# Performance work log

Hardware: AMD Instinct MI355X
Metric: run time of the kernel (lower is better)

The kernel has to match this reference:

```python
import jax, jax.numpy as jnp
import numpy as np

B, CIN, COUT, K, H, W = 16, 128, 256, 3, 56, 56
STRIDE = 1
PAD = K // 2


def setup_inputs() -> dict:
    key = jax.random.key(0)
    ks = jax.random.split(key, 12)
    x = jax.random.normal(ks[0], (B, CIN, H, W), dtype=jnp.float32)
    base_kernel = jax.random.normal(ks[1], (COUT, CIN, K, K), dtype=jnp.float32)
    bias = jnp.zeros((COUT,), dtype=jnp.float32)
    s = 1.0 / np.sqrt(CIN)
    fc_spatial_w = jax.random.uniform(ks[2], (K * K, CIN), minval=-s, maxval=s)
    fc_spatial_b = jax.random.uniform(ks[3], (K * K,), minval=-s, maxval=s)
    fc_in_w = jax.random.uniform(ks[4], (CIN, CIN), minval=-s, maxval=s)
    fc_in_b = jax.random.uniform(ks[5], (CIN,), minval=-s, maxval=s)
    fc_out_w = jax.random.uniform(ks[6], (COUT, CIN), minval=-s, maxval=s)
    fc_out_b = jax.random.uniform(ks[7], (COUT,), minval=-s, maxval=s)
    fc_kernel_w = jax.random.uniform(ks[8], (COUT * CIN * K * K, CIN), minval=-s, maxval=s)
    fc_kernel_b = jax.random.uniform(ks[9], (COUT * CIN * K * K,), minval=-s, maxval=s)
    return {
        "x": x, "base_kernel": base_kernel, "bias": bias,
        "fc_spatial_w": fc_spatial_w, "fc_spatial_b": fc_spatial_b,
        "fc_in_w": fc_in_w, "fc_in_b": fc_in_b,
        "fc_out_w": fc_out_w, "fc_out_b": fc_out_b,
        "fc_kernel_w": fc_kernel_w, "fc_kernel_b": fc_kernel_b,
    }


def _odconv(x, base_kernel, bias, fc_spatial_w, fc_spatial_b, fc_in_w, fc_in_b,
            fc_out_w, fc_out_b, fc_kernel_w, fc_kernel_b):
    b = x.shape[0]
    # global average pool -> context [B, Cin]
    context = jnp.mean(x, axis=(2, 3))
    sig = jax.nn.sigmoid
    attn_spatial = sig(context @ fc_spatial_w.T + fc_spatial_b).reshape(b, 1, 1, K, K)
    attn_in = sig(context @ fc_in_w.T + fc_in_b).reshape(b, 1, CIN, 1, 1)
    attn_out = sig(context @ fc_out_w.T + fc_out_b).reshape(b, COUT, 1, 1, 1)
    attn_kernel = sig(context @ fc_kernel_w.T + fc_kernel_b).reshape(b, COUT, CIN, K, K)
    # 5-way broadcast multiply -> per-sample dynamic kernel [B, Cout, Cin, K, K]
    dyn = base_kernel[None] * attn_out * attn_in * attn_spatial * attn_kernel

    def conv_one(xi, wi):
        # xi: [Cin, H, W], wi: [Cout, Cin, K, K]
        out = jax.lax.conv_general_dilated(
            xi[None], wi,
            window_strides=(STRIDE, STRIDE),
            padding=[(PAD, PAD), (PAD, PAD)],
            dimension_numbers=("NCHW", "OIHW", "NCHW"),
        )
        return out[0]

    out = jax.vmap(conv_one)(x, dyn)  # [B, Cout, H', W']
    return out + bias[None, :, None, None]


def reference(x, base_kernel, bias, fc_spatial_w, fc_spatial_b, fc_in_w, fc_in_b,
              fc_out_w, fc_out_b, fc_kernel_w, fc_kernel_b):
    return _odconv(x, base_kernel, bias, fc_spatial_w, fc_spatial_b, fc_in_w, fc_in_b,
                   fc_out_w, fc_out_b, fc_kernel_w, fc_kernel_b)
```

## Files before the change

kernel.cpp:

```cpp
#include <hip/hip_runtime.h>
#include <hip/hip_bf16.h>
#include <math.h>

#define BATCH 16
#define CIN   128
#define COUT  256
#define HH    56
#define WW    56
#define HW    3136
#define NTAP  9
#define NE    (COUT*CIN*NTAP)

typedef short short8 __attribute__((ext_vector_type(8)));
typedef float floatx4 __attribute__((ext_vector_type(4)));

#define WSB_CTX   0
#define WSB_ASP   8192
#define WSB_AIN   9472
#define WSB_AOUT  17664
#define WSB_ZP    34048
#define WSB_XT    38144
#define WSB_DYN   (WSB_XT + BATCH*HW*CIN*2)

static __device__ inline unsigned short f2b(float f) {
    union { float f; unsigned u; } v; v.f = f;
    unsigned r = v.u + 0x7FFF + ((v.u >> 16) & 1);
    return (unsigned short)(r >> 16);
}
static __device__ inline short8 pack8(float4 a, float4 b) {
    short8 r;
    r[0] = (short)f2b(a.x); r[1] = (short)f2b(a.y); r[2] = (short)f2b(a.z); r[3] = (short)f2b(a.w);
    r[4] = (short)f2b(b.x); r[5] = (short)f2b(b.y); r[6] = (short)f2b(b.z); r[7] = (short)f2b(b.w);
    return r;
}

typedef const __attribute__((address_space(1))) void* gas_ptr;
typedef __attribute__((address_space(3))) void* las_ptr;
static __device__ __forceinline__ void gl_lds16(const void* g, void* l) {
    __builtin_amdgcn_global_load_lds((gas_ptr)g, (las_ptr)l, 16, 0, 0);
}

__global__ void k_context(const float* __restrict__ x, float* __restrict__ ctx,
                          float* __restrict__ zp) {
    int bc = blockIdx.x;
    if (bc == 0 && threadIdx.x < 64) {
        uint4 z = {0u, 0u, 0u, 0u};
        ((uint4*)zp)[threadIdx.x] = z;
    }
    const float4* p = (const float4*)(x + (size_t)bc * HW);
    float s = 0.f;
    for (int i = threadIdx.x; i < HW / 4; i += 256) { float4 v = p[i]; s += v.x + v.y + v.z + v.w; }
    for (int off = 32; off; off >>= 1) s += __shfl_down(s, off, 64);
    __shared__ float red[4];
    if ((threadIdx.x & 63) == 0) red[threadIdx.x >> 6] = s;
    __syncthreads();
    if (threadIdx.x == 0) ctx[bc] = (red[0] + red[1] + red[2] + red[3]) * (1.f / (float)HW);
}

__global__ void k_attn(const float* __restrict__ ctx,
                       const float* __restrict__ wsp, const float* __restrict__ bsp,
                       const float* __restrict__ win, const float* __restrict__ bin,
                       const float* __restrict__ wout, const float* __restrict__ bout,
                       float* __restrict__ asp, float* __restrict__ ain, float* __restrict__ aout) {
    int R = blockIdx.x * 4 + (threadIdx.x >> 6);
    int lane = threadIdx.x & 63;
    int b = R / 393, r = R % 393;
    const float* w; float bias; float* o;
    if (r < 9)        { w = wsp  + r * CIN;         bias = bsp[r];         o = asp  + b * 16  + r; }
    else if (r < 137) { w = win  + (r - 9) * CIN;   bias = bin[r - 9];     o = ain  + b * CIN + (r - 9); }
    else              { w = wout + (r - 137) * CIN; bias = bout[r - 137];  o = aout + b * COUT + (r - 137); }
    float2 wv = ((const float2*)w)[lane];
    float2 cv = ((const float2*)(ctx + b * CIN))[lane];
    float d = wv.x * cv.x + wv.y * cv.y;
    for (int off = 32; off; off >>= 1) d += __shfl_down(d, off, 64);
    if (lane == 0) *o = 1.f / (1.f + __expf(-(d + bias)));
}

#define XT_BLOCKS    784
#define BUILD_BLOCKS 1152
__global__ void k_fat(const float* __restrict__ x, unsigned short* __restrict__ xt,
                      const float* __restrict__ ctx, const float* __restrict__ wk,
                      const float* __restrict__ bk, const float* __restrict__ base,
                      const float* __restrict__ asp, const float* __restrict__ ain,
                      const float* __restrict__ aout, unsigned short* __restrict__ dyn) {
    if (blockIdx.x < XT_BLOCKS) {
        int bid = blockIdx.x;
        int b = bid / 49;
        int p = (bid % 49) * 64 + (threadIdx.x & 63);
        int icq = threadIdx.x >> 6;
        const float* xb = x + (size_t)b * CIN * HW + p;
        unsigned short tmp[32];
#pragma unroll
        for (int j = 0; j < 32; ++j) tmp[j] = f2b(xb[(size_t)(icq * 32 + j) * HW]);
        uint4* dst = (uint4*)(xt + ((size_t)b * HW + p) * CIN + icq * 32);
        const uint4* s = (const uint4*)tmp;
        dst[0] = s[0]; dst[1] = s[1]; dst[2] = s[2]; dst[3] = s[3];
        return;
    }
    int bid = blockIdx.x - XT_BLOCKS;
    int wid = threadIdx.x >> 6, l = threadIdx.x & 63;
    int lq = l & 15, quad = l >> 4;
    short8 afr[4];
    const float* arow = ctx + lq * CIN;
#pragma unroll
    for (int kc = 0; kc < 4; ++kc) {
        float4 v0 = *(const float4*)(arow + kc * 32 + quad * 8);
        float4 v1 = *(const float4*)(arow + kc * 32 + quad * 8 + 4);
        afr[kc] = pack8(v0, v1);
    }
    int n0w = bid * 256 + wid * 64;
    for (int nf = 0; nf < 4; ++nf) {
        int n0 = n0w + nf * 16;
        int ic  = (n0 & 127) + lq;
        int oc  = (n0 >> 7) & 255;
        int tap = n0 >> 15;
        int e = (oc * CIN + ic) * NTAP + tap;
        const float* wrow = wk + (size_t)e * CIN;
        floatx4 acc = {0.f, 0.f, 0.f, 0.f};
#pragma unroll
        for (int kc = 0; kc < 4; ++kc) {
            float4 v0 = *(const float4*)(wrow + kc * 32 + quad * 8);
            float4 v1 = *(const float4*)(wrow + kc * 32 + quad * 8 + 4);
            short8 bfr = pack8(v0, v1);
            acc = __builtin_amdgcn_mfma_f32_16x16x32_bf16(afr[kc], bfr, acc, 0, 0, 0);
        }
        float bke = bk[e], bse = base[e];
#pragma unroll
        for (int r = 0; r < 4; ++r) {
            int b = quad * 4 + r;
            float s = 1.f / (1.f + __expf(-(acc[r] + bke)));
            float v = bse * s * aout[b * COUT + oc] * ain[b * CIN + ic] * asp[b * 16 + tap];
            dyn[(size_t)b * NE + n0 + lq] = f2b(v);
        }
    }
}

__global__ __launch_bounds__(256, 2) void k_conv(
    const unsigned short* __restrict__ xt, const unsigned short* __restrict__ dyn,
    const float* __restrict__ bias, float* __restrict__ out,
    const unsigned short* __restrict__ zp) {
    __shared__ char s_x[640 * 64];
    __shared__ char s_a[576 * 64];
    int id  = blockIdx.x;
    int low = id & 7;
    int q   = id >> 3;
    int r   = q % 7;
    int phi = q / 7;
    int p   = phi * 8 + low;
    int oc0 = (p >> 4) * 64;
    int b   = p & 15;
    int r0  = r * 8;

    int tid = threadIdx.x;
    int wn = tid >> 6, l = tid & 63, lq = l & 15, quad = l >> 4;
    const unsigned short* xtb  = xt  + (size_t)b * HW * CIN;
    const unsigned short* dynb = dyn + (size_t)b * NE;

    int colx = wn * 16 + (l >> 2);
    int gxs  = colx - 1;
    bool gxok = (unsigned)gxs < (unsigned)WW;
    const unsigned short* zsrc = zp + l * 8;

    int pixaddr[7];
#pragma unroll
    for (int nf = 0; nf < 7; ++nf) {
        int n = nf * 16 + lq;
        int tr = wn * 2 + n / 56, col = n % 56;
        pixaddr[nf] = (tr * 64 + col) * 64 + quad * 16;
    }

    floatx4 acc[4][7];
#pragma unroll
    for (int i = 0; i < 4; ++i)
#pragma unroll
        for (int j = 0; j < 7; ++j) acc[i][j] = (floatx4){0.f, 0.f, 0.f, 0.f};

    for (int kc = 0; kc < 4; ++kc) {
        __syncthreads();
#pragma unroll
        for (int ry = 0; ry < 10; ++ry) {
            int gy = r0 + ry - 1;
            const unsigned short* src =
                (gxok && (unsigned)gy < (unsigned)HH)
                    ? xtb + (size_t)(gy * WW + gxs) * CIN + kc * 32 + (l & 3) * 8
                    : zsrc;
            gl_lds16(src, s_x + ry * 4096 + wn * 1024);
        }
#pragma unroll
        for (int i = 0; i < 9; ++i) {
            int u = i * 256 + tid;
            int icq2 = u & 3, oc = (u >> 2) & 63, tap = u >> 8;
            gl_lds16(dynb + (size_t)(tap * COUT + oc0 + oc) * CIN + kc * 32 + icq2 * 8,
                     s_a + i * 4096 + wn * 1024);
        }
        __syncthreads();
        __builtin_amdgcn_s_setprio(1);
#pragma unroll
        for (int tap = 0; tap < 9; ++tap) {
            short8 af[4];
#pragma unroll
            for (int mf = 0; mf < 4; ++mf)
                af[mf] = *(const short8*)(s_a + (tap * 64 + mf * 16 + lq) * 64 + quad * 16);
            int toff = (tap / 3) * 4096 + (tap % 3) * 64;
#pragma unroll
            for (int nf = 0; nf < 7; ++nf) {
                short8 bf = *(const short8*)(s_x + pixaddr[nf] + toff);
#pragma unroll
                for (int mf = 0; mf < 4; ++mf)
                    acc[mf][nf] = __builtin_amdgcn_mfma_f32_16x16x32_bf16(af[mf], bf, acc[mf][nf], 0, 0, 0);
            }
        }
        __builtin_amdgcn_s_setprio(0);
    }

#pragma unroll
    for (int mf = 0; mf < 4; ++mf) {
#pragma unroll
        for (int rr = 0; rr < 4; ++rr) {
            int oc = oc0 + mf * 16 + quad * 4 + rr;
            float bs = bias[oc];
            float* ob = out + (size_t)(b * COUT + oc) * HW + (r0 + wn * 2) * 56 + lq;
#pragma unroll
            for (int nf = 0; nf < 7; ++nf)
                ob[nf * 16] = acc[mf][nf][rr] + bs;
        }
    }
}

extern "C" void kernel_launch(void* const* d_in, const int* in_sizes, int n_in,
                              void* d_out, int out_size, void* d_ws, size_t ws_size,
                              hipStream_t stream) {
    const float* x    = (const float*)d_in[0];
    const float* base = (const float*)d_in[1];
    const float* bias = (const float*)d_in[2];
    const float* wsp  = (const float*)d_in[3];
    const float* bsp  = (const float*)d_in[4];
    const float* win  = (const float*)d_in[5];
    const float* bin  = (const float*)d_in[6];
    const float* wout = (const float*)d_in[7];
    const float* bout = (const float*)d_in[8];
    const float* wk   = (const float*)d_in[9];
    const float* bk   = (const float*)d_in[10];
    float* out = (float*)d_out;
    char* ws = (char*)d_ws;

    float* ctx  = (float*)(ws + WSB_CTX);
    float* asp  = (float*)(ws + WSB_ASP);
    float* ain  = (float*)(ws + WSB_AIN);
    float* aout = (float*)(ws + WSB_AOUT);
    float* zp   = (float*)(ws + WSB_ZP);
    unsigned short* xt  = (unsigned short*)(ws + WSB_XT);
    unsigned short* dyn = (unsigned short*)(ws + WSB_DYN);

    k_context<<<BATCH * CIN, 256, 0, stream>>>(x, ctx, zp);
    k_attn<<<(BATCH * 393) / 4, 256, 0, stream>>>(ctx, wsp, bsp, win, bin, wout, bout, asp, ain, aout);
    k_fat<<<XT_BLOCKS + BUILD_BLOCKS, 256, 0, stream>>>(x, xt, ctx, wk, bk, base, asp, ain, aout, dyn);
    k_conv<<<448, 256, 0, stream>>>(xt, dyn, bias, out, (const unsigned short*)zp);
}
```

Before: 313.3 us.

## Read fc_kernel_w rows contiguously and transpose dyn results through LDS

The dynamic-kernel build blocks now take 256 contiguous element indices of fc_kernel_w instead of a tap-major slice. The old slice read weight rows strided by nine. Each wave issues all of its B-fragment loads before running its MFMAs, which raises memory-level parallelism. Results go to a shared-memory buffer indexed by tap, batch and site, then are written back as short runs in the tap-major dyn layout. This trades fully coalesced dyn stores and an added barrier and LDS traffic for sequential reads of the large weight matrix.

```diff
diff --git a/kernel.cpp b/kernel.cpp
--- a/kernel.cpp
+++ b/kernel.cpp
@@ -83,6 +83,7 @@
                       const float* __restrict__ bk, const float* __restrict__ base,
                       const float* __restrict__ asp, const float* __restrict__ ain,
                       const float* __restrict__ aout, unsigned short* __restrict__ dyn) {
+    __shared__ unsigned short s_res[9 * 530 + 16];
     if (blockIdx.x < XT_BLOCKS) {
         int bid = blockIdx.x;
         int b = bid / 49;
@@ -100,6 +101,9 @@
     int bid = blockIdx.x - XT_BLOCKS;
     int wid = threadIdx.x >> 6, l = threadIdx.x & 63;
     int lq = l & 15, quad = l >> 4;
+    int e0      = bid * 256;
+    int siteMin = e0 / 9;
+
     short8 afr[4];
     const float* arow = ctx + lq * CIN;
 #pragma unroll
@@ -108,29 +112,57 @@
         float4 v1 = *(const float4*)(arow + kc * 32 + quad * 8 + 4);
         afr[kc] = pack8(v0, v1);
     }
-    int n0w = bid * 256 + wid * 64;
-    for (int nf = 0; nf < 4; ++nf) {
-        int n0 = n0w + nf * 16;
-        int ic  = (n0 & 127) + lq;
-        int oc  = (n0 >> 7) & 255;
-        int tap = n0 >> 15;
-        int e = (oc * CIN + ic) * NTAP + tap;
+
+    int ebase = e0 + wid * 64;
+    short8 bfr[4][4];
+    float bke[4], bse[4];
+#pragma unroll
+    for (int j = 0; j < 4; ++j) {
+        unsigned e = ebase + j * 16 + lq;
         const float* wrow = wk + (size_t)e * CIN;
-        floatx4 acc = {0.f, 0.f, 0.f, 0.f};
 #pragma unroll
         for (int kc = 0; kc < 4; ++kc) {
             float4 v0 = *(const float4*)(wrow + kc * 32 + quad * 8);
             float4 v1 = *(const float4*)(wrow + kc * 32 + quad * 8 + 4);
-            short8 bfr = pack8(v0, v1);
-            acc = __builtin_amdgcn_mfma_f32_16x16x32_bf16(afr[kc], bfr, acc, 0, 0, 0);
-        }
-        float bke = bk[e], bse = base[e];
+            bfr[j][kc] = pack8(v0, v1);
+        }
+        bke[j] = bk[e]; bse[j] = base[e];
+    }
+    floatx4 acc[4];
+#pragma unroll
+    for (int j = 0; j < 4; ++j) acc[j] = (floatx4){0.f, 0.f, 0.f, 0.f};
+#pragma unroll
+    for (int j = 0; j < 4; ++j)
+#pragma unroll
+        for (int kc = 0; kc < 4; ++kc)
+            acc[j] = __builtin_amdgcn_mfma_f32_16x16x32_bf16(afr[kc], bfr[j][kc], acc[j], 0, 0, 0);
+#pragma unroll
+    for (int j = 0; j < 4; ++j) {
+        unsigned e = ebase + j * 16 + lq;
+        unsigned site = e / 9u, tap = e - site * 9u;
+        unsigned oc = site >> 7, ic = site & 127;
+        unsigned ds = site - siteMin;
 #pragma unroll
         for (int r = 0; r < 4; ++r) {
             int b = quad * 4 + r;
-            float s = 1.f / (1.f + __expf(-(acc[r] + bke)));
-            float v = bse * s * aout[b * COUT + oc] * ain[b * CIN + ic] * asp[b * 16 + tap];
-            dyn[(size_t)b * NE + n0 + lq] = f2b(v);
+            float s = 1.f / (1.f + __expf(-(acc[j][r] + bke[j])));
+            float v = bse[j] * s * aout[b * COUT + oc] * ain[b * CIN + ic] * asp[b * 16 + tap];
+            s_res[tap * 530 + b * 32 + ds] = f2b(v);
+        }
+    }
+    __syncthreads();
+    int hw_id = threadIdx.x >> 5;
+    int hl    = threadIdx.x & 31;
+#pragma unroll
+    for (int it = 0; it < 18; ++it) {
+        int pair = it * 8 + hw_id;
+        int t = pair >> 4, b = pair & 15;
+        int sLo = (e0 - t + 8) / 9;
+        int sHi = (e0 + 255 - t) / 9;
+        int cnt = sHi - sLo + 1;
+        if (hl < cnt) {
+            unsigned short v = s_res[t * 530 + b * 32 + (sLo - siteMin) + hl];
+            dyn[(size_t)b * NE + t * 32768 + sLo + hl] = v;
         }
     }
 }
```

After: 313.9 us. Within noise of the previous version (+0.2%).
